# Kernel optimization log

Hardware: AMD Instinct MI355X
Metric: run time of the kernel (lower is better)

## Reference

```python
import jax, jax.numpy as jnp
import numpy as np

# yolov5 non_max_suppression defaults (from forward's input_parameters.get defaults)
CONF_THRES = 0.25
IOU_THRES = 0.45
MAX_DET = 1000        # max detections returned per image
TOP_K = 4096          # fixed candidate count entering greedy NMS (jit-friendly stand-in for max_nms)
MAX_WH = 7680.0       # per-class box offset so NMS is class-aware (yolov5 trick)


def setup_inputs() -> dict:
    key = jax.random.key(0)
    k1, k2, k3, k4 = jax.random.split(key, 4)
    B, N, NC = 16, 25200, 80  # 640x640 yolov5 -> 25200 anchors, 80 COCO classes
    xy = jax.random.uniform(k1, (B, N, 2)) * 640.0            # box centers in pixels
    wh = jax.random.uniform(k2, (B, N, 2)) * 160.0 + 4.0       # box sizes
    obj = jax.random.uniform(k3, (B, N, 1))                    # objectness
    cls = jax.random.uniform(k4, (B, N, NC))                   # class scores
    pred = jnp.concatenate([xy, wh, obj, cls], axis=-1)        # [B, N, 85]
    return {"pred": pred}


def _xywh2xyxy(x):
    xy, wh = x[..., :2], x[..., 2:4]
    return jnp.concatenate([xy - wh * 0.5, xy + wh * 0.5], axis=-1)


def _iou_one_vs_all(box, boxes):
    # box [4], boxes [K,4], xyxy
    lt = jnp.maximum(box[:2], boxes[:, :2])
    rb = jnp.minimum(box[2:], boxes[:, 2:])
    wh = jnp.clip(rb - lt, 0.0)
    inter = wh[:, 0] * wh[:, 1]
    a1 = (box[2] - box[0]) * (box[3] - box[1])
    a2 = (boxes[:, 2] - boxes[:, 0]) * (boxes[:, 3] - boxes[:, 1])
    return inter / (a1 + a2 - inter + 1e-7)


def _nms_single(pred):
    # pred [N, 5+nc] raw yolov5 output for one image
    obj = pred[:, 4:5]
    scores_all = pred[:, 5:] * obj                 # conf = obj_conf * cls_conf
    conf = scores_all.max(axis=-1)                 # best-class confidence [N]
    cls = scores_all.argmax(axis=-1).astype(pred.dtype)
    boxes = _xywh2xyxy(pred[:, :4])                # [N,4] xyxy

    valid = conf > CONF_THRES
    s = jnp.where(valid, conf, -1.0)
    order = jnp.argsort(-s)[:TOP_K]                # top candidates by score
    b = boxes[order]                               # [K,4]
    sc = s[order]                                  # [K]
    c = cls[order]                                 # [K]
    ob = b + c[:, None] * MAX_WH                   # class-offset boxes for class-aware NMS

    ar = jnp.arange(TOP_K)

    def step(supp, i):
        alive = (~supp[i]) & (sc[i] > 0.0)
        iou = _iou_one_vs_all(ob[i], ob)
        supp = supp | (alive & (iou > IOU_THRES) & (ar > i))
        return supp, alive

    _, keep = jax.lax.scan(step, jnp.zeros(TOP_K, dtype=bool), ar)

    fs = jnp.where(keep, sc, -1.0)
    idx = jnp.argsort(-fs)[:MAX_DET]               # kept boxes, score-sorted
    det = jnp.concatenate([b[idx], fs[idx][:, None], c[idx][:, None]], axis=-1)  # [max_det,6]
    ok = fs[idx] > 0.0
    return jnp.where(ok[:, None], det, 0.0)        # zero-padded [max_det, 6] (x1,y1,x2,y2,conf,cls)


def reference(pred):
    # [B, max_det, 6] padded detections per image
    return jax.vmap(_nms_single)(pred)
```

## Files before the change

kernel.cpp:

```cpp
#include <hip/hip_runtime.h>

#define BATCH  16
#define NPRED  25200
#define NCLS   80
#define CDIM   85
#define TOPK   4096
#define NBUCK  4096
#define MAXDET 1000
#define CONF_T 0.25f
#define IOU_T  0.45f
#define MAXWH  7680.0f
#define ORD_BASE 0xBE800000u

typedef unsigned long long u64;
typedef unsigned int u32;
typedef unsigned short u16;
typedef unsigned char u8;

__device__ __forceinline__ u64 umax64(u64 a, u64 b) { return a > b ? a : b; }
__device__ __forceinline__ u64 umin64(u64 a, u64 b) { return a < b ? a : b; }

__device__ __forceinline__ void cx_u64(u64* a, int i, int p, bool desc) {
    u64 x = a[i], y = a[p];
    if (desc ? (x < y) : (x > y)) { a[i] = y; a[p] = x; }
}


__device__ void hybrid_sort4096_desc(u64 r[4], u64* a) {
    const int tid = threadIdx.x;
    for (int k = 2; k <= 4096; k <<= 1) {
        if (k >= 512) {
            int jmax = (k >> 1) > 2048 ? 2048 : (k >> 1);
#pragma unroll
            for (int e = 0; e < 4; ++e) a[4 * tid + e] = r[e];
            __syncthreads();
            for (int j = jmax; j >= 256; j >>= 1) {
#pragma unroll
                for (int t2 = 0; t2 < 2; ++t2) {
                    int q = (t2 << 10) | tid;
                    int i = ((q & ~(j - 1)) << 1) | (q & (j - 1));
                    cx_u64(a, i, i | j, (i & k) == 0);
                }
                __syncthreads();
            }
#pragma unroll
            for (int e = 0; e < 4; ++e) r[e] = a[4 * tid + e];
            __syncthreads();
        }
        {
            int jstart = (k >> 1) > 128 ? 128 : (k >> 1);
            bool desc = (((4 * tid) & k) == 0);
            for (int j = jstart; j >= 4; j >>= 1) {
                int m = j >> 2;
                bool take_max = (((tid & m) == 0) == desc);
#pragma unroll
                for (int e = 0; e < 4; ++e) {
                    u64 v = __shfl_xor(r[e], m, 64);
                    r[e] = take_max ? umax64(r[e], v) : umin64(r[e], v);
                }
            }
        }
        if (k >= 4) {
            bool desc = (((4 * tid) & k) == 0);
            u64 x0 = r[0], x2 = r[2];
            r[0] = desc ? umax64(x0, x2) : umin64(x0, x2);
            r[2] = desc ? umin64(x0, x2) : umax64(x0, x2);
            u64 x1 = r[1], x3 = r[3];
            r[1] = desc ? umax64(x1, x3) : umin64(x1, x3);
            r[3] = desc ? umin64(x1, x3) : umax64(x1, x3);
        }
        {
            bool d01 = (((4 * tid + 0) & k) == 0);
            bool d23 = (((4 * tid + 2) & k) == 0);
            u64 x0 = r[0], x1 = r[1];
            r[0] = d01 ? umax64(x0, x1) : umin64(x0, x1);
            r[1] = d01 ? umin64(x0, x1) : umax64(x0, x1);
            u64 x2 = r[2], x3 = r[3];
            r[2] = d23 ? umax64(x2, x3) : umin64(x2, x3);
            r[3] = d23 ? umin64(x2, x3) : umax64(x2, x3);
        }
    }
}

__device__ void wave_sort256_desc(u64 r[4]) {
    const int lane = threadIdx.x & 63;
    for (int k = 2; k <= 256; k <<= 1) {
        int jstart = (k >> 1) > 128 ? 128 : (k >> 1);
        bool desc = (((4 * lane) & k) == 0);
        for (int j = jstart; j >= 4; j >>= 1) {
            int m = j >> 2;
            bool take_max = (((lane & m) == 0) == desc);
#pragma unroll
            for (int e = 0; e < 4; ++e) {
                u64 v = __shfl_xor(r[e], m, 64);
                r[e] = take_max ? umax64(r[e], v) : umin64(r[e], v);
            }
        }
        if (k >= 4) {
            u64 x0 = r[0], x2 = r[2];
            r[0] = desc ? umax64(x0, x2) : umin64(x0, x2);
            r[2] = desc ? umin64(x0, x2) : umax64(x0, x2);
            u64 x1 = r[1], x3 = r[3];
            r[1] = desc ? umax64(x1, x3) : umin64(x1, x3);
            r[3] = desc ? umin64(x1, x3) : umax64(x1, x3);
        }
        {
            bool d01 = (((4 * lane + 0) & k) == 0);
            bool d23 = (((4 * lane + 2) & k) == 0);
            u64 x0 = r[0], x1 = r[1];
            r[0] = d01 ? umax64(x0, x1) : umin64(x0, x1);
            r[1] = d01 ? umin64(x0, x1) : umax64(x0, x1);
            u64 x2 = r[2], x3 = r[3];
            r[2] = d23 ? umax64(x2, x3) : umin64(x2, x3);
            r[3] = d23 ? umin64(x2, x3) : umax64(x2, x3);
        }
    }
}


__global__ __launch_bounds__(256) void k1_score(const float* __restrict__ pred,
                                                u64* __restrict__ keys,
                                                u32* __restrict__ ghist) {
    const int lane = threadIdx.x & 63;
    const int l16 = lane & 15;
    const long long gw = (long long)blockIdx.x * 4 + (threadIdx.x >> 6);
    const long long rowIdx = gw * 4 + (lane >> 4);
    const int b = (int)(rowIdx / NPRED);
    const int n = (int)(rowIdx - (long long)b * NPRED);
    const float* row = pred + rowIdx * CDIM;
    float obj = row[4];
    u64 m = 0ull;
#pragma unroll
    for (int k = 0; k < 5; ++k) {
        int c = l16 + 16 * k;
        float v = row[5 + c] * obj;
        u64 mk = ((u64)(__float_as_uint(v) | 0x80000000u) << 32) | (u64)(u32)(NCLS - 1 - c);
        if (mk > m) m = mk;
    }
#pragma unroll
    for (int o = 8; o > 0; o >>= 1) {
        u64 other = __shfl_xor(m, o, 64);
        if (other > m) m = other;
    }
    if (l16 == 0) {
        float best = __uint_as_float((u32)(m >> 32) & 0x7FFFFFFFu);
        int cls = (NCLS - 1) - (int)(m & 0x7Fu);
        float s = (best > CONF_T) ? best : -1.0f;
        u32 u = __float_as_uint(s);
        u32 ord = (u & 0x80000000u) ? ~u : (u | 0x80000000u);
        keys[rowIdx] = ((u64)ord << 32) | ((u64)(u32)(32767 - n) << 7) | (u64)(u32)cls;
        if (ord > ORD_BASE)
            atomicAdd(&ghist[b * NBUCK + ((ord - ORD_BASE - 1u) >> 12)], 1u);
    }
}


__global__ __launch_bounds__(1024) void k2cs(const u64* __restrict__ keys,
                                             const u32* __restrict__ ghist,
                                             u64* __restrict__ topSorted) {
    __shared__ u64 smem[4096];
    __shared__ u64 side[1024];
    __shared__ u32 wsum[16];
    __shared__ int sh_T, sh_C1, sh_R, c1pos, sidepos;
    const int b = blockIdx.x;
    const int tid = threadIdx.x;
    const int lane = tid & 63;
    const int wid = tid >> 6;
    const u64 lanelt = (1ull << lane) - 1ull;

    u32 h[4];
    u32 tsum = 0;
#pragma unroll
    for (int e = 0; e < 4; ++e) {
        h[e] = ghist[b * NBUCK + (NBUCK - 1 - (4 * tid + e))];
        tsum += h[e];
    }
    u32 inc = tsum;
    for (int o = 1; o < 64; o <<= 1) {
        u32 v = __shfl_up(inc, o, 64);
        if (lane >= o) inc += v;
    }
    if (lane == 63) wsum[wid] = inc;
    __syncthreads();
    if (tid == 0) {
        u32 run = 0;
        for (int i = 0; i < 16; ++i) { u32 t = wsum[i]; wsum[i] = run; run += t; }
        sh_T = -1; sh_C1 = (int)run; sh_R = 0;
        c1pos = 0; sidepos = 0;
    }
    __syncthreads();
    {
        u32 cum = wsum[wid] + (inc - tsum);
#pragma unroll
        for (int e = 0; e < 4; ++e) {
            if (h[e] > 0 && cum < (u32)TOPK && cum + h[e] >= (u32)TOPK) {
                sh_T = NBUCK - 1 - (4 * tid + e);
                sh_C1 = (int)cum;
                sh_R = TOPK - (int)cum;
            }
            cum += h[e];
        }
    }
    __syncthreads();
    const int T = sh_T, C1 = sh_C1, R = sh_R;

    for (int i = tid; i < 4096; i += 1024) smem[i] = 0ull;
    side[tid] = 0ull;
    __syncthreads();
    const u64* kb = keys + (long long)b * NPRED;
    for (int it = 0; it < (NPRED + 1023) / 1024; ++it) {
        int n = it * 1024 + tid;
        bool act = n < NPRED;
        u64 key = act ? kb[n] : 0ull;
        u32 hi = (u32)(key >> 32);
        bool v = act && (hi > ORD_BASE);
        int bt = v ? (int)((hi - ORD_BASE - 1u) >> 12) : -1;
        bool t1 = v && (bt > T);
        bool t2 = v && (bt == T);
        u64 m1 = __ballot(t1), m2 = __ballot(t2);
        int b1 = 0, b2 = 0;
        if (lane == 0) {
            if (m1) b1 = atomicAdd(&c1pos, (int)__popcll(m1));
            if (m2) b2 = atomicAdd(&sidepos, (int)__popcll(m2));
        }
        b1 = __shfl(b1, 0, 64);
        b2 = __shfl(b2, 0, 64);
        if (t1) smem[b1 + __popcll(m1 & lanelt)] = key;
        if (t2) { int s2 = b2 + __popcll(m2 & lanelt); if (s2 < 1024) side[s2] = key; }
    }
    __syncthreads();

    if (R > 0) {
        int cntT = sidepos;
        if (cntT <= 256) {
            if (wid == 0) {
                u64 r[4];
#pragma unroll
                for (int e = 0; e < 4; ++e) r[e] = side[4 * lane + e];
                wave_sort256_desc(r);
#pragma unroll
                for (int e = 0; e < 4; ++e) side[4 * lane + e] = r[e];
            }
        } else {
            for (int k = 2; k <= 1024; k <<= 1) {
                for (int j = k >> 1; j >= 1; j >>= 1) {
                    if (tid < 512) {
                        int q = tid;
                        int i = ((q & ~(j - 1)) << 1) | (q & (j - 1));
                        cx_u64(side, i, i | j, (i & k) == 0);
                    }
                    __syncthreads();
                }
            }
        }
        __syncthreads();
        if (tid < R) smem[C1 + tid] = side[tid];
    }
    __syncthreads();

    u64 r[4];
#pragma unroll
    for (int e = 0; e < 4; ++e) r[e] = smem[4 * tid + e];
    hybrid_sort4096_desc(r, smem);
#pragma unroll
    for (int e = 0; e < 4; ++e) topSorted[(long long)b * TOPK + 4 * tid + e] = r[e];
}


__global__ __launch_bounds__(64) void k3_nms(const float* __restrict__ pred,
                                             const u64* __restrict__ topSorted,
                                             u8* __restrict__ keep) {
    const int b = blockIdx.x;
    const int c = blockIdx.y;
    const int lane = threadIdx.x;
    __shared__ u32 list[4096];
    __shared__ float4 sbox[1024];
    __shared__ u8 suppb[4096];
    const u64* tb = topSorted + (long long)b * TOPK;
    const u64 lanelt = (1ull << lane) - 1ull;

    u32 pos = 0;
    for (int it = 0; it < 64; ++it) {
        u64 key = tb[it * 64 + lane];
        u32 hi = (u32)(key >> 32);
        bool mine = (hi > 0x80000000u) && ((int)(key & 0x7Fu) == c);
        u64 m = __ballot(mine);
        if (mine)
            list[pos + __popcll(m & lanelt)] =
                ((u32)(it * 64 + lane) << 15) | (32767u - (u32)((key >> 7) & 0x7FFFu));
        pos += (u32)__popcll(m);
    }
    const int n = (int)pos;
    if (n == 0) return;
    u8* kb = keep + b * TOPK;
    const float off = (float)c * MAXWH;

    if (n <= 128) {
        u32 r0 = 0, r1 = 0;
        float4 b0 = make_float4(0.0f, 0.0f, 0.0f, 0.0f);
        float4 b1 = make_float4(0.0f, 0.0f, 0.0f, 0.0f);
        if (lane < n) {
            u32 e = list[lane];
            r0 = e >> 15;
            const float* row = pred + ((long long)b * NPRED + (int)(e & 0x7FFFu)) * CDIM;
            float x = row[0], y = row[1], w = row[2], hh = row[3];
            b0.x = (x - w * 0.5f) + off;
            b0.y = (y - hh * 0.5f) + off;
            b0.z = (x + w * 0.5f) + off;
            b0.w = (y + hh * 0.5f) + off;
        }
        if (64 + lane < n) {
            u32 e = list[64 + lane];
            r1 = e >> 15;
            const float* row = pred + ((long long)b * NPRED + (int)(e & 0x7FFFu)) * CDIM;
            float x = row[0], y = row[1], w = row[2], hh = row[3];
            b1.x = (x - w * 0.5f) + off;
            b1.y = (y - hh * 0.5f) + off;
            b1.z = (x + w * 0.5f) + off;
            b1.w = (y + hh * 0.5f) + off;
        }
        {
#pragma clang fp contract(off)
            float a20 = (b0.z - b0.x) * (b0.w - b0.y);
            float a21 = (b1.z - b1.x) * (b1.w - b1.y);
            u64 rem0 = (n >= 64) ? ~0ull : ((1ull << n) - 1ull);
            u64 rem1 = (n > 64) ? ((n >= 128) ? ~0ull : ((1ull << (n - 64)) - 1ull)) : 0ull;
            u64 keep0 = 0ull, keep1 = 0ull;
            const bool two = (n > 64);
            while (rem0) {
                int ii = __builtin_ctzll(rem0);
                rem0 &= ~(1ull << ii);
                keep0 |= 1ull << ii;
                float bix = __shfl(b0.x, ii, 64);
                float biy = __shfl(b0.y, ii, 64);
                float biz = __shfl(b0.z, ii, 64);
                float biw = __shfl(b0.w, ii, 64);
                float a1  = __shfl(a20, ii, 64);
                {
                    float ltx = fmaxf(bix, b0.x), lty = fmaxf(biy, b0.y);
                    float rbx = fminf(biz, b0.z), rby = fminf(biw, b0.w);
                    float ww = fmaxf(rbx - ltx, 0.0f), hh = fmaxf(rby - lty, 0.0f);
                    float inter = ww * hh;
                    float iou = inter / (((a1 + a20) - inter) + 1e-7f);
                    bool k0 = (iou > IOU_T) && (lane > ii);
                    rem0 &= ~__ballot(k0);
                }
                if (two) {
                    float ltx = fmaxf(bix, b1.x), lty = fmaxf(biy, b1.y);
                    float rbx = fminf(biz, b1.z), rby = fminf(biw, b1.w);
                    float ww = fmaxf(rbx - ltx, 0.0f), hh = fmaxf(rby - lty, 0.0f);
                    float inter = ww * hh;
                    float iou = inter / (((a1 + a21) - inter) + 1e-7f);
                    bool k1 = (iou > IOU_T);
                    rem1 &= ~__ballot(k1);
                }
            }
            while (rem1) {
                int ii = __builtin_ctzll(rem1);
                rem1 &= ~(1ull << ii);
                keep1 |= 1ull << ii;
                float bix = __shfl(b1.x, ii, 64);
                float biy = __shfl(b1.y, ii, 64);
                float biz = __shfl(b1.z, ii, 64);
                float biw = __shfl(b1.w, ii, 64);
                float a1  = __shfl(a21, ii, 64);
                float ltx = fmaxf(bix, b1.x), lty = fmaxf(biy, b1.y);
                float rbx = fminf(biz, b1.z), rby = fminf(biw, b1.w);
                float ww = fmaxf(rbx - ltx, 0.0f), hh = fmaxf(rby - lty, 0.0f);
                float inter = ww * hh;
                float iou = inter / (((a1 + a21) - inter) + 1e-7f);
                bool k1 = (iou > IOU_T) && (lane > ii);
                rem1 &= ~__ballot(k1);
            }
            if ((keep0 >> lane) & 1ull) kb[r0] = 1;
            if ((keep1 >> lane) & 1ull) kb[r1] = 1;
        }
    } else {
        for (int j = lane; j < 1024; j += 64) {
            if (j < n) {
                u32 e = list[j];
                const float* row = pred + ((long long)b * NPRED + (int)(e & 0x7FFFu)) * CDIM;
                float x = row[0], y = row[1], w = row[2], hh = row[3];
                float4 o;
                o.x = (x - w * 0.5f) + off;
                o.y = (y - hh * 0.5f) + off;
                o.z = (x + w * 0.5f) + off;
                o.w = (y + hh * 0.5f) + off;
                sbox[j] = o;
            }
        }
        for (int j = lane; j < n; j += 64) suppb[j] = 0;
        __syncthreads();
        volatile u8* supp = suppb;
        {
#pragma clang fp contract(off)
            for (int ii = 0; ii < n; ++ii) {
                if (supp[ii]) continue;
                u32 ei = list[ii];
                int ri = (int)(ei >> 15);
                if (lane == 0) kb[ri] = 1;
                float4 bi;
                if (ii < 1024) bi = sbox[ii];
                else {
                    const float* row = pred + ((long long)b * NPRED + (int)(ei & 0x7FFFu)) * CDIM;
                    float x = row[0], y = row[1], w = row[2], hh = row[3];
                    bi.x = (x - w * 0.5f) + off;
                    bi.y = (y - hh * 0.5f) + off;
                    bi.z = (x + w * 0.5f) + off;
                    bi.w = (y + hh * 0.5f) + off;
                }
                float a1 = (bi.z - bi.x) * (bi.w - bi.y);
                for (int jj = ii + 1 + lane; jj < n; jj += 64) {
                    float4 bj;
                    if (jj < 1024) bj = sbox[jj];
                    else {
                        u32 ej = list[jj];
                        const float* row = pred + ((long long)b * NPRED + (int)(ej & 0x7FFFu)) * CDIM;
                        float x = row[0], y = row[1], w = row[2], hh = row[3];
                        bj.x = (x - w * 0.5f) + off;
                        bj.y = (y - hh * 0.5f) + off;
                        bj.z = (x + w * 0.5f) + off;
                        bj.w = (y + hh * 0.5f) + off;
                    }
                    float ltx = fmaxf(bi.x, bj.x), lty = fmaxf(bi.y, bj.y);
                    float rbx = fminf(bi.z, bj.z), rby = fminf(bi.w, bj.w);
                    float ww = fmaxf(rbx - ltx, 0.0f), hh = fmaxf(rby - lty, 0.0f);
                    float inter = ww * hh;
                    float a2 = (bj.z - bj.x) * (bj.w - bj.y);
                    float iou = inter / (((a1 + a2) - inter) + 1e-7f);
                    if (iou > IOU_T) supp[jj] = 1;
                }
                __syncthreads();
            }
        }
    }
}


__global__ __launch_bounds__(256) void k4_out(const float* __restrict__ pred,
                                              const u64* __restrict__ topSorted,
                                              const u8* __restrict__ keep,
                                              float* __restrict__ out) {
    const int b = blockIdx.x;
    const int tid = threadIdx.x;
    __shared__ u64 words[64];
    __shared__ int wpre[64];
    float* outb = out + (long long)b * MAXDET * 6;
    for (int i = tid; i < MAXDET * 6; i += 256) outb[i] = 0.0f;
    const u8* kp = keep + b * 4096;
    if (tid < 64) {
        u64 w = 0ull;
        const u64* k8 = (const u64*)(kp + tid * 64);
#pragma unroll
        for (int q = 0; q < 8; ++q) {
            u64 v = k8[q];
#pragma unroll
            for (int bb = 0; bb < 8; ++bb)
                if ((v >> (8 * bb)) & 0xFFull) w |= 1ull << (q * 8 + bb);
        }
        words[tid] = w;
    }
    __syncthreads();
    if (tid == 0) {
        int run = 0;
        for (int t = 0; t < 64; ++t) { wpre[t] = run; run += __popcll(words[t]); }
    }
    __syncthreads();
    const u64* kb = topSorted + (long long)b * TOPK;
    for (int r = tid; r < 4096; r += 256) {
        int wd = r >> 6;
        if ((words[wd] >> (r & 63)) & 1ull) {
            int pos = wpre[wd] + __popcll(words[wd] & ((1ull << (r & 63)) - 1ull));
            if (pos < MAXDET) {
                u64 key = kb[r];
                u32 hi = (u32)(key >> 32);
                int n = 32767 - (int)((key >> 7) & 0x7FFFu);
                const float* row = pred + ((long long)b * NPRED + n) * CDIM;
                float x = row[0], y = row[1], w2 = row[2], h = row[3];
                float* o = outb + pos * 6;
                o[0] = x - w2 * 0.5f;
                o[1] = y - h * 0.5f;
                o[2] = x + w2 * 0.5f;
                o[3] = y + h * 0.5f;
                o[4] = __uint_as_float(hi & 0x7FFFFFFFu);
                o[5] = (float)(key & 0x7Fu);
            }
        }
    }
}


extern "C" void kernel_launch(void* const* d_in, const int* in_sizes, int n_in,
                              void* d_out, int out_size, void* d_ws, size_t ws_size,
                              hipStream_t stream) {
    const float* pred = (const float*)d_in[0];
    float* out = (float*)d_out;

    char* ws = (char*)d_ws;
    u64* keys      = (u64*)ws;
    u64* topSorted = (u64*)(ws + 3225600);
    u32* ghist     = (u32*)(ws + 3749888);
    u8*  keep      = (u8*)(ws + 4012032);
    (void)hipMemsetAsync(ws + 3749888, 0, 327680, stream);

    hipLaunchKernelGGL(k1_score, dim3(BATCH * NPRED / 16), dim3(256), 0, stream,
                       pred, keys, ghist);
    hipLaunchKernelGGL(k2cs, dim3(BATCH), dim3(1024), 0, stream, keys, ghist, topSorted);
    hipLaunchKernelGGL(k3_nms, dim3(BATCH, NCLS), dim3(64), 0, stream,
                       pred, topSorted, keep);
    hipLaunchKernelGGL(k4_out, dim3(BATCH), dim3(256), 0, stream, pred, topSorted, keep, out);
}
```

Measured before the change: 291.4 us.

## Move histogram to shared memory and split top-K sort across more blocks

The per-image score histogram is now built in shared memory inside the selection kernel, which removes the global atomics in the scoring kernel and the memset. The 4096-key bitonic sort is split in two. 64 blocks each sort 1024-key chunks in alternating directions, then a per-image kernel runs only the final merge stages starting at k=2048. This spreads the sort over more CUs, at the cost of two extra launches and a global round trip of the candidate buffer. The keep buffer is now zeroed inside k2a.

Result: no change. 286.0 us (-1.8%).

```diff
diff --git a/kernel.cpp b/kernel.cpp
--- a/kernel.cpp
+++ b/kernel.cpp
@@ -26,9 +26,9 @@
 }
 
 
-__device__ void hybrid_sort4096_desc(u64 r[4], u64* a) {
+__device__ void hybrid_sort4096_desc_ks(u64 r[4], u64* a, int kstart) {
     const int tid = threadIdx.x;
-    for (int k = 2; k <= 4096; k <<= 1) {
+    for (int k = kstart; k <= 4096; k <<= 1) {
         if (k >= 512) {
             int jmax = (k >> 1) > 2048 ? 2048 : (k >> 1);
 #pragma unroll
@@ -82,6 +82,63 @@
     }
 }
 
+
+__device__ void hybrid_sort1024_dir(u64 r[4], u64* a, bool fdesc) {
+    const int tid = threadIdx.x;
+    for (int k = 2; k <= 1024; k <<= 1) {
+        if (k >= 512) {
+            int jmax = (k >> 1) > 512 ? 512 : (k >> 1);
+#pragma unroll
+            for (int e = 0; e < 4; ++e) a[4 * tid + e] = r[e];
+            __syncthreads();
+            for (int j = jmax; j >= 256; j >>= 1) {
+#pragma unroll
+                for (int t2 = 0; t2 < 2; ++t2) {
+                    int q = (t2 << 8) | tid;
+                    int i = ((q & ~(j - 1)) << 1) | (q & (j - 1));
+                    cx_u64(a, i, i | j, ((i & k) == 0) == fdesc);
+                }
+                __syncthreads();
+            }
+#pragma unroll
+            for (int e = 0; e < 4; ++e) r[e] = a[4 * tid + e];
+            __syncthreads();
+        }
+        {
+            int jstart = (k >> 1) > 128 ? 128 : (k >> 1);
+            bool desc = ((((4 * tid) & k) == 0) == fdesc);
+            for (int j = jstart; j >= 4; j >>= 1) {
+                int m = j >> 2;
+                bool take_max = (((tid & m) == 0) == desc);
+#pragma unroll
+                for (int e = 0; e < 4; ++e) {
+                    u64 v = __shfl_xor(r[e], m, 64);
+                    r[e] = take_max ? umax64(r[e], v) : umin64(r[e], v);
+                }
+            }
+        }
+        if (k >= 4) {
+            bool desc = ((((4 * tid) & k) == 0) == fdesc);
+            u64 x0 = r[0], x2 = r[2];
+            r[0] = desc ? umax64(x0, x2) : umin64(x0, x2);
+            r[2] = desc ? umin64(x0, x2) : umax64(x0, x2);
+            u64 x1 = r[1], x3 = r[3];
+            r[1] = desc ? umax64(x1, x3) : umin64(x1, x3);
+            r[3] = desc ? umin64(x1, x3) : umax64(x1, x3);
+        }
+        {
+            bool d01 = ((((4 * tid + 0) & k) == 0) == fdesc);
+            bool d23 = ((((4 * tid + 2) & k) == 0) == fdesc);
+            u64 x0 = r[0], x1 = r[1];
+            r[0] = d01 ? umax64(x0, x1) : umin64(x0, x1);
+            r[1] = d01 ? umin64(x0, x1) : umax64(x0, x1);
+            u64 x2 = r[2], x3 = r[3];
+            r[2] = d23 ? umax64(x2, x3) : umin64(x2, x3);
+            r[3] = d23 ? umin64(x2, x3) : umax64(x2, x3);
+        }
+    }
+}
+
 __device__ void wave_sort256_desc(u64 r[4]) {
     const int lane = threadIdx.x & 63;
     for (int k = 2; k <= 256; k <<= 1) {
@@ -119,8 +176,7 @@
 
 
 __global__ __launch_bounds__(256) void k1_score(const float* __restrict__ pred,
-                                                u64* __restrict__ keys,
-                                                u32* __restrict__ ghist) {
+                                                u64* __restrict__ keys) {
     const int lane = threadIdx.x & 63;
     const int l16 = lane & 15;
     const long long gw = (long long)blockIdx.x * 4 + (threadIdx.x >> 6);
@@ -149,17 +205,16 @@
         u32 u = __float_as_uint(s);
         u32 ord = (u & 0x80000000u) ? ~u : (u | 0x80000000u);
         keys[rowIdx] = ((u64)ord << 32) | ((u64)(u32)(32767 - n) << 7) | (u64)(u32)cls;
-        if (ord > ORD_BASE)
-            atomicAdd(&ghist[b * NBUCK + ((ord - ORD_BASE - 1u) >> 12)], 1u);
-    }
-}
-
-
-__global__ __launch_bounds__(1024) void k2cs(const u64* __restrict__ keys,
-                                             const u32* __restrict__ ghist,
-                                             u64* __restrict__ topSorted) {
+    }
+}
+
+
+__global__ __launch_bounds__(1024) void k2a(const u64* __restrict__ keys,
+                                            u64* __restrict__ topUn,
+                                            u8* __restrict__ keep) {
     __shared__ u64 smem[4096];
     __shared__ u64 side[1024];
+    __shared__ u32 hist[4096];
     __shared__ u32 wsum[16];
     __shared__ int sh_T, sh_C1, sh_R, c1pos, sidepos;
     const int b = blockIdx.x;
@@ -168,11 +223,27 @@
     const int wid = tid >> 6;
     const u64 lanelt = (1ull << lane) - 1ull;
 
+#pragma unroll
+    for (int e = 0; e < 4; ++e) { smem[4 * tid + e] = 0ull; hist[4 * tid + e] = 0u; }
+    side[tid] = 0ull;
+    ((u32*)keep)[b * 1024 + tid] = 0u;
+    __syncthreads();
+
+    const u64* kb = keys + (long long)b * NPRED;
+    for (int it = 0; it < (NPRED + 1023) / 1024; ++it) {
+        int n = it * 1024 + tid;
+        if (n < NPRED) {
+            u32 hi = (u32)(kb[n] >> 32);
+            if (hi > ORD_BASE) atomicAdd(&hist[(hi - ORD_BASE - 1u) >> 12], 1u);
+        }
+    }
+    __syncthreads();
+
     u32 h[4];
     u32 tsum = 0;
 #pragma unroll
     for (int e = 0; e < 4; ++e) {
-        h[e] = ghist[b * NBUCK + (NBUCK - 1 - (4 * tid + e))];
+        h[e] = hist[NBUCK - 1 - (4 * tid + e)];
         tsum += h[e];
     }
     u32 inc = tsum;
@@ -204,10 +275,6 @@
     __syncthreads();
     const int T = sh_T, C1 = sh_C1, R = sh_R;
 
-    for (int i = tid; i < 4096; i += 1024) smem[i] = 0ull;
-    side[tid] = 0ull;
-    __syncthreads();
-    const u64* kb = keys + (long long)b * NPRED;
     for (int it = 0; it < (NPRED + 1023) / 1024; ++it) {
         int n = it * 1024 + tid;
         bool act = n < NPRED;
@@ -258,10 +325,33 @@
     }
     __syncthreads();
 
+    for (int i = tid; i < 4096; i += 1024) topUn[(long long)b * TOPK + i] = smem[i];
+}
+
+
+__global__ __launch_bounds__(256) void k2b(u64* __restrict__ topUn) {
+    __shared__ u64 a[1024];
+    const int tid = threadIdx.x;
+    const int s = blockIdx.x & 3;
+    const long long base = (long long)blockIdx.x * 1024;
     u64 r[4];
 #pragma unroll
-    for (int e = 0; e < 4; ++e) r[e] = smem[4 * tid + e];
-    hybrid_sort4096_desc(r, smem);
+    for (int e = 0; e < 4; ++e) r[e] = topUn[base + 4 * tid + e];
+    hybrid_sort1024_dir(r, a, (s & 1) == 0);
+#pragma unroll
+    for (int e = 0; e < 4; ++e) topUn[base + 4 * tid + e] = r[e];
+}
+
+
+__global__ __launch_bounds__(1024) void k2c(const u64* __restrict__ topUn,
+                                            u64* __restrict__ topSorted) {
+    __shared__ u64 a[4096];
+    const int b = blockIdx.x;
+    const int tid = threadIdx.x;
+    u64 r[4];
+#pragma unroll
+    for (int e = 0; e < 4; ++e) r[e] = topUn[(long long)b * TOPK + 4 * tid + e];
+    hybrid_sort4096_desc_ks(r, a, 2048);
 #pragma unroll
     for (int e = 0; e < 4; ++e) topSorted[(long long)b * TOPK + 4 * tid + e] = r[e];
 }
@@ -498,14 +588,15 @@
 
     char* ws = (char*)d_ws;
     u64* keys      = (u64*)ws;
-    u64* topSorted = (u64*)(ws + 3225600);
-    u32* ghist     = (u32*)(ws + 3749888);
-    u8*  keep      = (u8*)(ws + 4012032);
-    (void)hipMemsetAsync(ws + 3749888, 0, 327680, stream);
+    u64* topUn     = (u64*)(ws + 3225600);
+    u64* topSorted = (u64*)(ws + 3749888);
+    u8*  keep      = (u8*)(ws + 4274176);
 
     hipLaunchKernelGGL(k1_score, dim3(BATCH * NPRED / 16), dim3(256), 0, stream,
-                       pred, keys, ghist);
-    hipLaunchKernelGGL(k2cs, dim3(BATCH), dim3(1024), 0, stream, keys, ghist, topSorted);
+                       pred, keys);
+    hipLaunchKernelGGL(k2a, dim3(BATCH), dim3(1024), 0, stream, keys, topUn, keep);
+    hipLaunchKernelGGL(k2b, dim3(BATCH * 4), dim3(256), 0, stream, topUn);
+    hipLaunchKernelGGL(k2c, dim3(BATCH), dim3(1024), 0, stream, topUn, topSorted);
     hipLaunchKernelGGL(k3_nms, dim3(BATCH, NCLS), dim3(64), 0, stream,
                        pred, topSorted, keep);
     hipLaunchKernelGGL(k4_out, dim3(BATCH), dim3(256), 0, stream, pred, topSorted, keep, out);
```
